# Kernel optimization log

Hardware: AMD Instinct MI355X
Metric: run time of the kernel (lower is better)

The kernel has to match this reference:

```python
import jax, jax.numpy as jnp
import numpy as np

HEADS = 8
DIM_HEAD = 64
CHUNK = 128
EPS = 1e-6
KERNEL_EPS = 1e-4


def softmax_kernel(x, proj, is_query):
    # x: [b,h,n,d], proj: [f,d]  (FAVOR+ positive softmax features)
    d = x.shape[-1]
    data_normalizer = d ** -0.25
    ratio = proj.shape[0] ** -0.5
    data_dash = jnp.einsum('bhnd,fd->bhnf', x * data_normalizer, proj)
    diag = 0.5 * (data_normalizer ** 2) * jnp.sum(x * x, axis=-1, keepdims=True)  # [b,h,n,1]
    if is_query:
        m = jnp.max(data_dash, axis=-1, keepdims=True)
    else:
        m = jnp.max(data_dash, axis=(-1, -2), keepdims=True)
    return ratio * (jnp.exp(data_dash - diag - jax.lax.stop_gradient(m)) + KERNEL_EPS)


def infer_hidden_states(q, k, v, chunk_size=CHUNK):
    # q,k: [b,h,n,f], v: [b,h,n,e]; chunked causal linear attention with carried cumsums
    b, h, n, f = q.shape
    e = v.shape[-1]
    nc = n // chunk_size

    def to_chunks(t):
        return jnp.moveaxis(t.reshape(b, h, nc, chunk_size, t.shape[-1]), 2, 0)

    qs, ks, vs = to_chunks(q), to_chunks(k), to_chunks(v)

    def step(carry, inp):
        Z, S = carry  # [b,h,1,f], [b,h,1,f,e]
        qc, kc, vc = inp
        k_cum = Z + jnp.cumsum(kc, axis=2)                       # [b,h,c,f]
        D_inv = 1.0 / jnp.einsum('bhnf,bhnf->bhn', qc, k_cum + EPS)
        ctx = jnp.einsum('bhnf,bhne->bhnfe', kc, vc)             # [b,h,c,f,e]
        ctx_cum = S + jnp.cumsum(ctx, axis=2)
        out = jnp.einsum('bhnfe,bhnf,bhn->bhne', ctx_cum, qc, D_inv)
        return (k_cum[:, :, -1:], ctx_cum[:, :, -1:]), out

    init = (jnp.zeros((b, h, 1, f), q.dtype), jnp.zeros((b, h, 1, f, e), q.dtype))
    (Z, S), outs = jax.lax.scan(step, init, (qs, ks, vs))
    out = jnp.moveaxis(outs, 0, 2).reshape(b, h, n, e)
    return out, Z[:, :, 0], S[:, :, 0]


def reference(x, proj, Wq, Wk, Wv, Wo, bo):
    b, n, dim = x.shape
    h, dh = HEADS, DIM_HEAD

    def split_heads(t):
        return jnp.transpose(t.reshape(b, n, h, dh), (0, 2, 1, 3))

    q = split_heads(x @ Wq)
    k = split_heads(x @ Wk)
    v = split_heads(x @ Wv)

    qf = softmax_kernel(q, proj, is_query=True)
    kf = softmax_kernel(k, proj, is_query=False)

    out, Z, S = infer_hidden_states(qf, kf, v)
    out = jnp.transpose(out, (0, 2, 1, 3)).reshape(b, n, h * dh)
    out = out @ Wo + bo
    return out, Z, S


def setup_inputs() -> dict:
    key = jax.random.key(0)
    ks = jax.random.split(key, 6)
    b, n, dim = 2, 2048, 512
    f = 256
    return {
        'x': jax.random.normal(ks[0], (b, n, dim), jnp.float32),
        'proj': jax.random.normal(ks[1], (f, DIM_HEAD), jnp.float32),
        'Wq': jax.random.normal(ks[2], (dim, dim), jnp.float32) * (dim ** -0.5),
        'Wk': jax.random.normal(ks[3], (dim, dim), jnp.float32) * (dim ** -0.5),
        'Wv': jax.random.normal(ks[4], (dim, dim), jnp.float32) * (dim ** -0.5),
        'Wo': jax.random.normal(ks[5], (dim, dim), jnp.float32) * (dim ** -0.5),
        'bo': jnp.zeros((dim,), jnp.float32),
    }
```

## Files before the change

kernel.cpp:

```cpp
#include <hip/hip_runtime.h>
#include <hip/hip_bf16.h>
#include <math.h>

#define NB    2
#define NSEQ  2048
#define DIMM  512
#define NH    8
#define DHd   64
#define FF    256
#define CHK   128
#define NCHK  16
#define NBH   16

typedef unsigned short ushort_t;
typedef __attribute__((ext_vector_type(8))) __bf16 bf16x8;
typedef __attribute__((ext_vector_type(4))) float floatx4;

__device__ __forceinline__ unsigned short f2bf(float x) {
    union { __hip_bfloat16 h; unsigned short u; } v;
    v.h = __float2bfloat16(x);
    return v.u;
}
__device__ __forceinline__ float bf2f(unsigned short u) {
    union { unsigned short u2[2]; float f; } v;
    v.u2[0] = 0; v.u2[1] = u;
    return v.f;
}
__device__ __forceinline__ unsigned enc_f(float x) {
    unsigned u = __float_as_uint(x);
    return (u & 0x80000000u) ? ~u : (u | 0x80000000u);
}
__device__ __forceinline__ float dec_f(unsigned e) {
    unsigned u = (e & 0x80000000u) ? (e & 0x7fffffffu) : ~e;
    return __uint_as_float(u);
}

__device__ __forceinline__ void gload16(const void* g, void* l) {
    __builtin_amdgcn_global_load_lds(
        (const __attribute__((address_space(1))) void*)g,
        (__attribute__((address_space(3))) void*)l, 16, 0, 0);
}

__device__ __forceinline__ bf16x8 frag8(const ushort_t* lds, int row, int kb) {
    return *((const bf16x8*)lds + row * 8 + (kb ^ (row & 7)));
}
__device__ __forceinline__ bf16x8 fragS(const ushort_t* lds, int row, int kb) {
    return *((const bf16x8*)lds + row * 16 + (kb ^ (row & 15)));
}

__device__ __forceinline__ void stage8(const ushort_t* __restrict__ G, ushort_t* dst,
                                       int ld, int tid) {
#pragma unroll
    for (int t = 0; t < 4; t++) {
        const int g = t * 256 + tid, r = g >> 3, kb = (g & 7) ^ (r & 7);
        gload16(G + (size_t)r * ld + kb * 8, dst + (size_t)g * 8);
    }
}
__device__ __forceinline__ void stage4h(const ushort_t* __restrict__ G, ushort_t* dst,
                                        int ld, int tid) {
#pragma unroll
    for (int t = 0; t < 2; t++) {
        const int g = t * 256 + tid, r = g >> 3, kb = (g & 7) ^ (r & 7);
        gload16(G + (size_t)r * ld + kb * 8, dst + (size_t)g * 8);
    }
}
__device__ __forceinline__ void stageV(const ushort_t* __restrict__ G, ushort_t* dst,
                                       int tid) {
#pragma unroll
    for (int t = 0; t < 4; t++) {
        const int g = t * 256 + tid, r = g >> 4, kb = (g & 15) ^ (r & 15);
        gload16(G + (size_t)r * NSEQ + kb * 8, dst + (size_t)g * 8);
    }
}

__global__ __launch_bounds__(256)
void prep(const float* __restrict__ x, const float* __restrict__ proj,
          const float* __restrict__ W0, const float* __restrict__ W1,
          const float* __restrict__ W2, const float* __restrict__ W3,
          ushort_t* __restrict__ xb, ushort_t* __restrict__ projb,
          ushort_t* __restrict__ T0, ushort_t* __restrict__ T1,
          ushort_t* __restrict__ T2, ushort_t* __restrict__ T3,
          unsigned* __restrict__ mk_u)
{
    __shared__ float t[32][33];
    const int b = blockIdx.x, tid = threadIdx.x;
    if (b < 2048) {
        const int gid = b * 256 + tid;
        const float4 v = *(const float4*)(x + (size_t)gid * 4);
        union { ushort4 v4; unsigned short s[4]; } pk;
        pk.s[0] = f2bf(v.x); pk.s[1] = f2bf(v.y); pk.s[2] = f2bf(v.z); pk.s[3] = f2bf(v.w);
        ((ushort4*)xb)[gid] = pk.v4;
    } else if (b < 2064) {
        const int gid = (b - 2048) * 256 + tid;
        const float dn = 0.35355339059327379f;
        const float4 v = *(const float4*)(proj + (size_t)gid * 4);
        union { ushort4 v4; unsigned short s[4]; } pk;
        pk.s[0] = f2bf(v.x * dn); pk.s[1] = f2bf(v.y * dn);
        pk.s[2] = f2bf(v.z * dn); pk.s[3] = f2bf(v.w * dn);
        ((ushort4*)projb)[gid] = pk.v4;
    } else if (b < 3088) {
        const int idx = b - 2064;
        const int z = idx >> 8, rem = idx & 255;
        const int bx = rem & 15, by = rem >> 4;
        const float* W = (z == 0) ? W0 : (z == 1) ? W1 : (z == 2) ? W2 : W3;
        ushort_t* T = (z == 0) ? T0 : (z == 1) ? T1 : (z == 2) ? T2 : T3;
        const int x0 = bx * 32, y0 = by * 32;
        const int tx = tid & 31, ty = tid >> 5;
#pragma unroll
        for (int i = 0; i < 4; i++)
            t[ty + i * 8][tx] = W[(size_t)(y0 + ty + i * 8) * DIMM + x0 + tx];
        __syncthreads();
#pragma unroll
        for (int i = 0; i < 4; i++)
            T[(size_t)(x0 + ty + i * 8) * DIMM + y0 + tx] = f2bf(t[tx][ty + i * 8]);
    } else {
        if (tid < NBH) mk_u[tid] = 0u;
    }
}

__device__ __forceinline__ void mfma_mainloop(
    const ushort_t* __restrict__ AG, const ushort_t* __restrict__ BG,
    ushort_t* As, ushort_t* Bs, int ldA, int ldB, int K,
    floatx4 acc[4][4], int tid)
{
    const int lane = tid & 63, wid = tid >> 6;
    const int q = lane >> 4, c = lane & 15;
    const int wm = (wid >> 1) * 64, wn = (wid & 1) * 64;

    for (int k0 = 0; k0 < K; k0 += 64) {
#pragma unroll
        for (int t = 0; t < 4; t++) {
            const int g = t * 256 + tid, r = g >> 3, kb = (g & 7) ^ (r & 7);
            gload16(AG + (size_t)r * ldA + k0 + kb * 8, As + (size_t)g * 8);
        }
#pragma unroll
        for (int t = 0; t < 4; t++) {
            const int g = t * 256 + tid, r = g >> 3, kb = (g & 7) ^ (r & 7);
            gload16(BG + (size_t)r * ldB + k0 + kb * 8, Bs + (size_t)g * 8);
        }
        __syncthreads();
#pragma unroll
        for (int ks = 0; ks < 2; ks++) {
            bf16x8 af[4], bfr[4];
#pragma unroll
            for (int i = 0; i < 4; i++) {
                af[i]  = frag8(As, wm + i * 16 + c, ks * 4 + q);
                bfr[i] = frag8(Bs, wn + i * 16 + c, ks * 4 + q);
            }
#pragma unroll
            for (int i = 0; i < 4; i++)
#pragma unroll
                for (int j = 0; j < 4; j++)
                    acc[i][j] = __builtin_amdgcn_mfma_f32_16x16x32_bf16(
                        af[i], bfr[j], acc[i][j], 0, 0, 0);
        }
        __syncthreads();
    }
}

__global__ __launch_bounds__(256)
void gemm_qkv(const ushort_t* __restrict__ xb,
              const ushort_t* __restrict__ Wtq, const ushort_t* __restrict__ Wtk,
              const ushort_t* __restrict__ Wtv, const ushort_t* __restrict__ projb,
              ushort_t* __restrict__ qb, ushort_t* __restrict__ kb,
              ushort_t* __restrict__ vTb, unsigned* __restrict__ mk_u)
{
    __shared__ alignas(16) ushort_t SM[25600];
    __shared__ float red[256];
    ushort_t* As = SM;
    ushort_t* Bs = SM + 8192;
    ushort_t* PS = SM + 17408;
    const int tid = threadIdx.x;
    const int bid = blockIdx.x;
    const int z = bid % 3, tt = bid / 3;
    const int n0 = (tt & 3) * 128, m0 = (tt >> 2) * 128;
    const ushort_t* Bt = (z == 0) ? Wtq : ((z == 1) ? Wtk : Wtv);

    floatx4 zero = {0.f, 0.f, 0.f, 0.f};
    floatx4 acc[4][4];
#pragma unroll
    for (int i = 0; i < 4; i++)
#pragma unroll
        for (int j = 0; j < 4; j++) acc[i][j] = zero;

    mfma_mainloop(xb + (size_t)m0 * DIMM, Bt + (size_t)n0 * DIMM, As, Bs,
                  DIMM, DIMM, DIMM, acc, tid);

    const int lane = tid & 63, wid = tid >> 6;
    const int q = lane >> 4, cl = lane & 15;
    const int wm = (wid >> 1) * 64, wn = (wid & 1) * 64;

#pragma unroll
    for (int i = 0; i < 4; i++)
#pragma unroll
        for (int j = 0; j < 4; j++) {
            const int col = wn + j * 16 + cl;
#pragma unroll
            for (int r = 0; r < 4; r++) {
                const int row = wm + i * 16 + q * 4 + r;
                SM[row * 136 + col] = f2bf(acc[i][j][r]);
            }
        }
    __syncthreads();

    if (z < 2) {
        ushort_t* ob = (z == 0) ? qb : kb;
        if (z == 1) {
#pragma unroll
            for (int t = 0; t < 4; t++) {
                const int g = t * 256 + tid, f = g >> 3, kbg = (g & 7) ^ (f & 7);
                gload16(projb + (size_t)f * 64 + kbg * 8, PS + (size_t)g * 8);
            }
        }
#pragma unroll
        for (int p = 0; p < 16; p++) {
            const int idx = p * 256 + tid;
            const int row = idx >> 5, c4 = idx & 31;
            ushort4 o = *(const ushort4*)&SM[row * 136 + c4 * 4];
            *(ushort4*)(ob + (size_t)(m0 + row) * DIMM + n0 + c4 * 4) = o;
        }
        if (z == 1) {
            const int bb = m0 >> 11;
            const int h0 = n0 >> 6;
            float mx[2] = {-3.0e38f, -3.0e38f};
#pragma unroll
            for (int half = 0; half < 2; half++) {
                __syncthreads();
#pragma unroll
                for (int hh = 0; hh < 2; hh++) {
                    floatx4 a2[4][4];
#pragma unroll
                    for (int i = 0; i < 4; i++)
#pragma unroll
                        for (int j = 0; j < 4; j++) a2[i][j] = zero;
#pragma unroll
                    for (int ks = 0; ks < 2; ks++) {
                        bf16x8 af[4], bfr[4];
#pragma unroll
                        for (int i = 0; i < 4; i++)
                            af[i] = *(const bf16x8*)&SM[(wm + i * 16 + cl) * 136 + hh * 64 + (ks * 4 + q) * 8];
#pragma unroll
                        for (int j = 0; j < 4; j++)
                            bfr[j] = frag8(PS, wn + j * 16 + cl, ks * 4 + q);
#pragma unroll
                        for (int i = 0; i < 4; i++)
#pragma unroll
                            for (int j = 0; j < 4; j++)
                                a2[i][j] = __builtin_amdgcn_mfma_f32_16x16x32_bf16(
                                    af[i], bfr[j], a2[i][j], 0, 0, 0);
                    }
#pragma unroll
                    for (int i = 0; i < 4; i++)
#pragma unroll
                        for (int j = 0; j < 4; j++)
#pragma unroll
                            for (int r = 0; r < 4; r++) mx[hh] = fmaxf(mx[hh], a2[i][j][r]);
                }
                if (half == 0) {
                    __syncthreads();
#pragma unroll
                    for (int t = 0; t < 4; t++) {
                        const int g = t * 256 + tid, f = g >> 3, kbg = (g & 7) ^ (f & 7);
                        gload16(projb + (size_t)(128 + f) * 64 + kbg * 8, PS + (size_t)g * 8);
                    }
                }
            }
#pragma unroll
            for (int hh = 0; hh < 2; hh++) {
                __syncthreads();
                red[tid] = mx[hh];
                __syncthreads();
                for (int s = 128; s > 0; s >>= 1) {
                    if (tid < s) red[tid] = fmaxf(red[tid], red[tid + s]);
                    __syncthreads();
                }
                if (tid == 0) atomicMax(&mk_u[bb * NH + h0 + hh], enc_f(red[0]));
            }
        }
    } else {
        const int bb = m0 >> 11, nbase = m0 & 2047;
#pragma unroll
        for (int p = 0; p < 16; p++) {
            const int idx = p * 256 + tid;
            const int cl2 = idx >> 5, n4 = idx & 31;
            const int C = n0 + cl2;
            const int h = C >> 6, e = C & 63;
            union { ushort4 v4; unsigned short s[4]; } pk;
#pragma unroll
            for (int k = 0; k < 4; k++) pk.s[k] = SM[(n4 * 4 + k) * 136 + cl2];
            *(ushort4*)(vTb + (((size_t)(bb * NH + h) * 64 + e)) * NSEQ + nbase + n4 * 4) = pk.v4;
        }
    }
}

__device__ __forceinline__ void mm24(const ushort_t* A, const ushort_t* B,
                                     floatx4 acc[2][4], int wm, int wn, int c, int q)
{
#pragma unroll
    for (int ks = 0; ks < 2; ks++) {
        bf16x8 af[2], bfr[4];
#pragma unroll
        for (int i = 0; i < 2; i++) af[i] = frag8(A, wm + i * 16 + c, ks * 4 + q);
#pragma unroll
        for (int j = 0; j < 4; j++) bfr[j] = frag8(B, wn + j * 16 + c, ks * 4 + q);
#pragma unroll
        for (int i = 0; i < 2; i++)
#pragma unroll
            for (int j = 0; j < 4; j++)
                acc[i][j] = __builtin_amdgcn_mfma_f32_16x16x32_bf16(
                    af[i], bfr[j], acc[i][j], 0, 0, 0);
    }
}

__global__ __launch_bounds__(256)
void gemm_out(const ushort_t* __restrict__ attnb, const ushort_t* __restrict__ Wto,
              float* __restrict__ out, const float* __restrict__ bias)
{
    __shared__ alignas(16) ushort_t A0[4096];
    __shared__ alignas(16) ushort_t A1[4096];
    __shared__ alignas(16) ushort_t B0[8192];
    __shared__ alignas(16) ushort_t B1[8192];
    const int tid = threadIdx.x;
    const int n0 = blockIdx.x * 128, m0 = blockIdx.y * 64;
    const ushort_t* AG = attnb + (size_t)m0 * DIMM;
    const ushort_t* BG = Wto + (size_t)n0 * DIMM;

    floatx4 zero = {0.f, 0.f, 0.f, 0.f};
    floatx4 acc[2][4];
#pragma unroll
    for (int i = 0; i < 2; i++)
#pragma unroll
        for (int j = 0; j < 4; j++) acc[i][j] = zero;

    const int lane = tid & 63, wid = tid >> 6;
    const int q = lane >> 4, c = lane & 15;
    const int wm = (wid >> 1) * 32, wn = (wid & 1) * 64;

    stage4h(AG, A0, DIMM, tid);
    stage8(BG, B0, DIMM, tid);
    __syncthreads();
    for (int tt = 0; tt < 4; tt++) {
        const int k0 = tt * 128;
        stage4h(AG + k0 + 64, A1, DIMM, tid);
        stage8(BG + k0 + 64, B1, DIMM, tid);
        mm24(A0, B0, acc, wm, wn, c, q);
        __syncthreads();
        if (tt < 3) {
            stage4h(AG + k0 + 128, A0, DIMM, tid);
            stage8(BG + k0 + 128, B0, DIMM, tid);
        }
        mm24(A1, B1, acc, wm, wn, c, q);
        __syncthreads();
    }

#pragma unroll
    for (int i = 0; i < 2; i++)
#pragma unroll
        for (int j = 0; j < 4; j++) {
            const int col = n0 + wn + j * 16 + c;
            const float bv = bias[col];
#pragma unroll
            for (int r = 0; r < 4; r++) {
                const int row = m0 + wm + i * 16 + q * 4 + r;
                out[(size_t)row * DIMM + col] = acc[i][j][r] + bv;
            }
        }
}

__global__ __launch_bounds__(256)
void featk(const ushort_t* __restrict__ kb_, const ushort_t* __restrict__ projb,
           const unsigned* __restrict__ mk_u, const ushort_t* __restrict__ vTb,
           ushort_t* __restrict__ kfb, float* __restrict__ CTXT,
           float* __restrict__ Ksum)
{
    __shared__ alignas(16) ushort_t SM[17408];
    __shared__ alignas(16) ushort_t Vs[8192];
    __shared__ float dtmp[256];
    __shared__ float diag_l[128];
    __shared__ float colp[2][128];
    ushort_t* As = SM;
    ushort_t* Bs = SM + 8192;
    const int tid = threadIdx.x, lane = tid & 63, wid = tid >> 6;
    const int q = lane >> 4, cl = lane & 15;
    const int m0 = blockIdx.x * 128, h = blockIdx.y, fh = blockIdx.z;
    const int bb = m0 >> 11, nloc = m0 & 2047;
    const int bh = bb * NH + h;
    const int cidx = nloc >> 7;
    const ushort_t* Aq = kb_ + (size_t)m0 * DIMM + h * 64;
    const ushort_t* Vg = vTb + ((size_t)bh * 64) * NSEQ + nloc;
    const ushort_t* Pj = projb + (size_t)fh * 128 * 64;

    {
        const int row = tid >> 1, half = tid & 1;
        float s = 0.f;
        const ushort_t* p = Aq + (size_t)row * DIMM + half * 32;
#pragma unroll
        for (int d = 0; d < 32; d += 4) {
            ushort4 w = *(const ushort4*)(p + d);
            float a = bf2f(w.x), b2 = bf2f(w.y), c2 = bf2f(w.z), d2 = bf2f(w.w);
            s += a * a + b2 * b2 + c2 * c2 + d2 * d2;
        }
        dtmp[tid] = s;
    }
    stage8(Aq, As, DIMM, tid);
    stage8(Pj, Bs, 64, tid);
    stageV(Vg, Vs, tid);
    __syncthreads();
    if (tid < 128) diag_l[tid] = (dtmp[2 * tid] + dtmp[2 * tid + 1]) * 0.0625f;

    floatx4 zero = {0.f, 0.f, 0.f, 0.f};
    floatx4 acc[4][4];
#pragma unroll
    for (int i = 0; i < 4; i++)
#pragma unroll
        for (int j = 0; j < 4; j++) acc[i][j] = zero;
    const int wm = (wid >> 1) * 64, wn = (wid & 1) * 64;
#pragma unroll
    for (int ks = 0; ks < 2; ks++) {
        bf16x8 af[4], bfr[4];
#pragma unroll
        for (int i = 0; i < 4; i++) af[i] = frag8(As, wm + i * 16 + cl, ks * 4 + q);
#pragma unroll
        for (int j = 0; j < 4; j++) bfr[j] = frag8(Bs, wn + j * 16 + cl, ks * 4 + q);
#pragma unroll
        for (int i = 0; i < 4; i++)
#pragma unroll
            for (int j = 0; j < 4; j++)
                acc[i][j] = __builtin_amdgcn_mfma_f32_16x16x32_bf16(
                    af[i], bfr[j], acc[i][j], 0, 0, 0);
    }
    __syncthreads();

    const float mk = dec_f(mk_u[bh]);
#pragma unroll
    for (int i = 0; i < 4; i++)
#pragma unroll
        for (int r = 0; r < 4; r++) {
            const int row = wm + i * 16 + q * 4 + r;
            const float cc = diag_l[row] + mk;
#pragma unroll
            for (int j = 0; j < 4; j++)
                acc[i][j][r] = 0.0625f * (__expf(acc[i][j][r] - cc) + 1.0e-4f);
        }

#pragma unroll
    for (int j = 0; j < 4; j++) {
        float s = 0.f;
#pragma unroll
        for (int i = 0; i < 4; i++)
            s += acc[i][j][0] + acc[i][j][1] + acc[i][j][2] + acc[i][j][3];
        s += __shfl_xor(s, 16);
        s += __shfl_xor(s, 32);
        if (q == 0) colp[wid >> 1][wn + j * 16 + cl] = s;
    }

#pragma unroll
    for (int i = 0; i < 4; i++)
#pragma unroll
        for (int j = 0; j < 4; j++) {
            const int col = wn + j * 16 + cl;
#pragma unroll
            for (int r = 0; r < 4; r++) {
                const int row = wm + i * 16 + q * 4 + r;
                SM[row * 136 + col] = f2bf(acc[i][j][r]);
            }
        }
    __syncthreads();

    if (tid < 128)
        Ksum[((size_t)bh * NCHK + cidx) * FF + fh * 128 + tid] = colp[0][tid] + colp[1][tid];

    const size_t frow = (size_t)bh * NSEQ + nloc;
#pragma unroll
    for (int p = 0; p < 16; p++) {
        const int idx = p * 256 + tid;
        const int row = idx >> 5, c4 = idx & 31;
        ushort4 o = *(const ushort4*)&SM[row * 136 + c4 * 4];
        *(ushort4*)(kfb + (frow + row) * FF + fh * 128 + c4 * 4) = o;
    }
    __syncthreads();

    ushort_t* T = SM;
    const size_t cbase = ((size_t)bh * NCHK + cidx) * 64;
#pragma unroll
    for (int fq = 0; fq < 2; fq++) {
        if ((wid & 1) == fq) {
#pragma unroll
            for (int jj = 0; jj < 4; jj++) {
#pragma unroll
                for (int i = 0; i < 4; i++)
#pragma unroll
                    for (int r = 0; r < 4; r++) {
                        const int n = wm + i * 16 + q * 4 + r;
                        T[(jj * 16 + cl) * 136 + n] = f2bf(acc[i][jj][r]);
                    }
            }
        }
        __syncthreads();
        floatx4 accc[4];
#pragma unroll
        for (int jj = 0; jj < 4; jj++) accc[jj] = zero;
#pragma unroll
        for (int kt = 0; kt < 4; kt++) {
            const bf16x8 av = fragS(Vs, wid * 16 + cl, kt * 4 + q);
#pragma unroll
            for (int jj = 0; jj < 4; jj++) {
                const bf16x8 bv = *(const bf16x8*)(T + (jj * 16 + cl) * 136 + (kt * 4 + q) * 8);
                accc[jj] = __builtin_amdgcn_mfma_f32_16x16x32_bf16(av, bv, accc[jj], 0, 0, 0);
            }
        }
#pragma unroll
        for (int jj = 0; jj < 4; jj++) {
            const int f = fh * 128 + fq * 64 + jj * 16 + cl;
#pragma unroll
            for (int r = 0; r < 4; r++) {
                const int e = wid * 16 + q * 4 + r;
                CTXT[(cbase + e) * FF + f] = accc[jj][r];
            }
        }
        __syncthreads();
    }
}

__global__ void prefix_zs(float* __restrict__ Ksum, float* __restrict__ Zout,
                          const float* __restrict__ CTXT, ushort_t* __restrict__ ctxp,
                          float* __restrict__ Sout)
{
    const int b = blockIdx.x;
    if (b < 1024) {
        const int idx = b * 256 + threadIdx.x;
        const int bh = idx >> 14, ef = idx & 16383;
        const int e = ef >> 8, f = ef & 255;
        float run = 0.f;
#pragma unroll
        for (int c = 0; c < NCHK; c++) {
            const size_t o = (((size_t)bh * NCHK + c) * 64 + e) * FF + f;
            const float t = CTXT[o];
            ctxp[o] = f2bf(run);
            run += t;
        }
        Sout[((size_t)bh * FF + f) * 64 + e] = run;
    } else {
        const int idx = (b - 1024) * 256 + threadIdx.x;
        const int bh = idx >> 8, f = idx & 255;
        float run = 0.f;
#pragma unroll
        for (int c = 0; c < NCHK; c++) {
            const size_t o = ((size_t)(bh * NCHK + c)) * FF + f;
            const float t = Ksum[o];
            Ksum[o] = run;
            run += t;
        }
        Zout[(size_t)bh * FF + f] = run;
    }
}

template<int NJ>
__device__ __forceinline__ void st1N(const ushort_t* QFs, const ushort_t* Bk,
                                     floatx4* acc1, int wv, int cl, int q)
{
#pragma unroll
    for (int ks = 0; ks < 2; ks++) {
        const bf16x8 af = frag8(QFs, wv * 16 + cl, ks * 4 + q);
        bf16x8 bfr[NJ];
#pragma unroll
        for (int j = 0; j < NJ; j++) bfr[j] = frag8(Bk, j * 16 + cl, ks * 4 + q);
#pragma unroll
        for (int j = 0; j < NJ; j++)
            acc1[j] = __builtin_amdgcn_mfma_f32_16x16x32_bf16(af, bfr[j], acc1[j], 0, 0, 0);
    }
}

__device__ __forceinline__ void pv4(const ushort_t* CpB, const ushort_t* QFs,
                                    floatx4 acc2[4], int wv, int cl, int q)
{
#pragma unroll
    for (int ks = 0; ks < 2; ks++) {
        const bf16x8 bfr = frag8(QFs, wv * 16 + cl, ks * 4 + q);
#pragma unroll
        for (int i = 0; i < 4; i++) {
            const bf16x8 af = frag8(CpB, i * 16 + cl, ks * 4 + q);
            acc2[i] = __builtin_amdgcn_mfma_f32_16x16x32_bf16(af, bfr, acc2[i], 0, 0, 0);
        }
    }
}

__global__ __launch_bounds__(256)
void chunk_out_half(const ushort_t* __restrict__ qb_, const ushort_t* __restrict__ projb,
                    const ushort_t* __restrict__ kfb, const ushort_t* __restrict__ vTb,
                    const float* __restrict__ Zex, const ushort_t* __restrict__ ctxp,
                    ushort_t* __restrict__ attnb)
{
    __shared__ alignas(16) ushort_t QF[16384];
    __shared__ alignas(16) ushort_t BufA[8192];
    __shared__ alignas(16) ushort_t Ssl[8192];
    __shared__ alignas(16) ushort_t BufB[4096];
    __shared__ float zeps[256];
    __shared__ float dtmp[256];
    __shared__ float diag_l[64];
    __shared__ float rows_part[64];
    __shared__ float denp[256];
    __shared__ float den_l[64];

    const int tid = threadIdx.x, lane = tid & 63, wv = tid >> 6;
    const int q = lane >> 4, cl = lane & 15;
    const int bh = blockIdx.x >> 5, r5 = blockIdx.x & 31;
    const int c = r5 >> 1, hq = r5 & 1;
    const int bb = bh >> 3, h = bh & 7;
    const int n0 = c * CHK, q0 = n0 + hq * 64;
    const ushort_t* Kf = kfb + ((size_t)bh * NSEQ + n0) * FF;
    const ushort_t* Aq = qb_ + ((size_t)(bb * NSEQ + q0)) * DIMM + h * 64;
    const ushort_t* Vt = vTb + ((size_t)bh * 64) * NSEQ + n0;
    const ushort_t* Cp = ctxp + ((size_t)bh * NCHK + c) * 64 * FF;

    zeps[tid] = Zex[((size_t)bh * NCHK + c) * FF + tid] + 1.0e-6f;

    stage4h(Aq, BufB, DIMM, tid);
    stage8(projb, BufA, 64, tid);
    stage8(projb + 128 * 64, Ssl, 64, tid);
    {
        const int row = tid >> 2, qd = tid & 3;
        float s = 0.f;
        const ushort_t* p = Aq + (size_t)row * DIMM + qd * 16;
#pragma unroll
        for (int d = 0; d < 16; d += 4) {
            ushort4 w = *(const ushort4*)(p + d);
            float a = bf2f(w.x), b2 = bf2f(w.y), c2 = bf2f(w.z), d2 = bf2f(w.w);
            s += a * a + b2 * b2 + c2 * c2 + d2 * d2;
        }
        dtmp[tid] = s;
    }
    __syncthreads();
    if (tid < 64)
        diag_l[tid] = (dtmp[4 * tid] + dtmp[4 * tid + 1] +
                       dtmp[4 * tid + 2] + dtmp[4 * tid + 3]) * 0.0625f;

    floatx4 zero = {0.f, 0.f, 0.f, 0.f};
    floatx4 accqA[8], accqB[8];
#pragma unroll
    for (int j = 0; j < 8; j++) { accqA[j] = zero; accqB[j] = zero; }
#pragma unroll
    for (int ks = 0; ks < 2; ks++) {
        const bf16x8 af = frag8(BufB, wv * 16 + cl, ks * 4 + q);
#pragma unroll
        for (int j = 0; j < 8; j++) {
            const bf16x8 b0 = frag8(BufA, j * 16 + cl, ks * 4 + q);
            accqA[j] = __builtin_amdgcn_mfma_f32_16x16x32_bf16(af, b0, accqA[j], 0, 0, 0);
        }
#pragma unroll
        for (int j = 0; j < 8; j++) {
            const bf16x8 b1 = frag8(Ssl, j * 16 + cl, ks * 4 + q);
            accqB[j] = __builtin_amdgcn_mfma_f32_16x16x32_bf16(af, b1, accqB[j], 0, 0, 0);
        }
    }
    float rmax[4];
#pragma unroll
    for (int r = 0; r < 4; r++) {
        float m = -3.0e38f;
#pragma unroll
        for (int j = 0; j < 8; j++) m = fmaxf(m, fmaxf(accqA[j][r], accqB[j][r]));
        m = fmaxf(m, __shfl_xor(m, 1)); m = fmaxf(m, __shfl_xor(m, 2));
        m = fmaxf(m, __shfl_xor(m, 4)); m = fmaxf(m, __shfl_xor(m, 8));
        rmax[r] = m;
    }
    __syncthreads();
#pragma unroll
    for (int r = 0; r < 4; r++) {
        const int rowL = wv * 16 + q * 4 + r;
        const float cc = diag_l[rowL] + rmax[r];
#pragma unroll
        for (int j = 0; j < 8; j++) {
            {
                const int col = j * 16 + cl;
                const float v = 0.0625f * (__expf(accqA[j][r] - cc) + 1.0e-4f);
                const int s = col >> 6, fp = col & 63;
                QF[s * 4096 + (rowL * 8 + ((fp >> 3) ^ (rowL & 7))) * 8 + (fp & 7)] = f2bf(v);
            }
            {
                const int col = 128 + j * 16 + cl;
                const float v = 0.0625f * (__expf(accqB[j][r] - cc) + 1.0e-4f);
                const int s = col >> 6, fp = col & 63;
                QF[s * 4096 + (rowL * 8 + ((fp >> 3) ^ (rowL & 7))) * 8 + (fp & 7)] = f2bf(v);
            }
        }
    }
    if (hq) stage8(Kf, Ssl, FF, tid); else stage4h(Kf, Ssl, FF, tid);
    __syncthreads();

    floatx4 acc1[8];
#pragma unroll
    for (int j = 0; j < 8; j++) acc1[j] = zero;
    if (hq) {
        stage8(Kf + 64, BufA, FF, tid);
        st1N<8>(QF, Ssl, acc1, wv, cl, q);
        __syncthreads();
        stage8(Kf + 128, Ssl, FF, tid);
        st1N<8>(QF + 4096, BufA, acc1, wv, cl, q);
        __syncthreads();
        stage8(Kf + 192, BufA, FF, tid);
        st1N<8>(QF + 8192, Ssl, acc1, wv, cl, q);
        __syncthreads();
        st1N<8>(QF + 12288, BufA, acc1, wv, cl, q);
    } else {
        stage4h(Kf + 64, BufA, FF, tid);
        st1N<4>(QF, Ssl, acc1, wv, cl, q);
        __syncthreads();
        stage4h(Kf + 128, Ssl, FF, tid);
        st1N<4>(QF + 4096, BufA, acc1, wv, cl, q);
        __syncthreads();
        stage4h(Kf + 192, BufA, FF, tid);
        st1N<4>(QF + 8192, Ssl, acc1, wv, cl, q);
        __syncthreads();
        st1N<4>(QF + 12288, BufA, acc1, wv, cl, q);
    }

    if (hq) {
#pragma unroll
        for (int r = 0; r < 4; r++) {
            const int rowL = wv * 16 + q * 4 + r;
            const int rowG = 64 + rowL;
            float part = 0.f;
#pragma unroll
            for (int j = 0; j < 8; j++) {
                const int col = j * 16 + cl;
                const float v = (col <= rowG) ? acc1[j][r] : 0.f;
                part += v;
                Ssl[(rowL * 16 + ((col >> 3) ^ (rowL & 15))) * 8 + (col & 7)] = f2bf(v);
            }
            part += __shfl_xor(part, 1); part += __shfl_xor(part, 2);
            part += __shfl_xor(part, 4); part += __shfl_xor(part, 8);
            if (cl == 0) rows_part[rowL] = part;
        }
    } else {
#pragma unroll
        for (int r = 0; r < 4; r++) {
            const int rowL = wv * 16 + q * 4 + r;
            float part = 0.f;
#pragma unroll
            for (int j = 0; j < 4; j++) {
                const int col = j * 16 + cl;
                const float v = (col <= rowL) ? acc1[j][r] : 0.f;
                part += v;
                Ssl[(rowL * 16 + ((col >> 3) ^ (rowL & 15))) * 8 + (col & 7)] = f2bf(v);
            }
            part += __shfl_xor(part, 1); part += __shfl_xor(part, 2);
            part += __shfl_xor(part, 4); part += __shfl_xor(part, 8);
            if (cl == 0) rows_part[rowL] = part;
        }
    }
    __syncthreads();

    if (hq) stageV(Vt, BufA, tid); else stage4h(Vt, BufA, NSEQ, tid);
    stage4h(Cp, BufB, FF, tid);
    float dacc = 0.f;
    {
        const int drow = tid >> 2, dq = tid & 3;
        const ushort_t* QQ = QF + dq * 4096;
#pragma unroll
        for (int gi = 0; gi < 8; gi++) {
            const ushort_t* gp = QQ + ((size_t)drow * 8 + (gi ^ (drow & 7))) * 8;
            const int kbase = dq * 64 + gi * 8;
#pragma unroll
            for (int e2 = 0; e2 < 8; e2++)
                dacc = fmaf(bf2f(gp[e2]), zeps[kbase + e2], dacc);
        }
    }
    __syncthreads();

    floatx4 acc2[4];
#pragma unroll
    for (int i = 0; i < 4; i++) acc2[i] = zero;
    if (hq) {
#pragma unroll
        for (int kk = 0; kk < 4; kk++) {
            const bf16x8 bfr = fragS(Ssl, wv * 16 + cl, kk * 4 + q);
#pragma unroll
            for (int i = 0; i < 4; i++) {
                const bf16x8 af = fragS(BufA, i * 16 + cl, kk * 4 + q);
                acc2[i] = __builtin_amdgcn_mfma_f32_16x16x32_bf16(af, bfr, acc2[i], 0, 0, 0);
            }
        }
    } else {
#pragma unroll
        for (int kk = 0; kk < 2; kk++) {
            const bf16x8 bfr = fragS(Ssl, wv * 16 + cl, kk * 4 + q);
#pragma unroll
            for (int i = 0; i < 4; i++) {
                const bf16x8 af = frag8(BufA, i * 16 + cl, kk * 4 + q);
                acc2[i] = __builtin_amdgcn_mfma_f32_16x16x32_bf16(af, bfr, acc2[i], 0, 0, 0);
            }
        }
    }
    denp[tid] = dacc;
    __syncthreads();

    stage4h(Cp + 64, BufA, FF, tid);
    stage4h(Cp + 128, BufA + 4096, FF, tid);
    pv4(BufB, QF, acc2, wv, cl, q);
    __syncthreads();
    stage4h(Cp + 192, BufB, FF, tid);
    pv4(BufA, QF + 4096, acc2, wv, cl, q);
    pv4(BufA + 4096, QF + 8192, acc2, wv, cl, q);
    if (tid < 64)
        den_l[tid] = rows_part[tid] + denp[4 * tid] + denp[4 * tid + 1] +
                     denp[4 * tid + 2] + denp[4 * tid + 3];
    __syncthreads();
    pv4(BufB, QF + 12288, acc2, wv, cl, q);

    const float dinv = 1.0f / den_l[wv * 16 + cl];
#pragma unroll
    for (int i = 0; i < 4; i++)
#pragma unroll
        for (int r = 0; r < 4; r++) {
            const int e = i * 16 + q * 4 + r;
            Ssl[(wv * 16 + cl) * 68 + e] = f2bf(acc2[i][r] * dinv);
        }
    __syncthreads();
#pragma unroll
    for (int p = 0; p < 4; p++) {
        const int idx = p * 256 + tid;
        const int row = idx >> 4, e4 = idx & 15;
        ushort4 o = *(const ushort4*)&Ssl[row * 68 + e4 * 4];
        *(ushort4*)(attnb + ((size_t)(bb * NSEQ + q0 + row)) * DIMM + h * 64 + e4 * 4) = o;
    }
}

extern "C" void kernel_launch(void* const* d_in, const int* in_sizes, int n_in,
                              void* d_out, int out_size, void* d_ws, size_t ws_size,
                              hipStream_t stream)
{
    (void)in_sizes; (void)n_in; (void)out_size; (void)ws_size;
    const float* x    = (const float*)d_in[0];
    const float* proj = (const float*)d_in[1];
    const float* Wq   = (const float*)d_in[2];
    const float* Wk   = (const float*)d_in[3];
    const float* Wv   = (const float*)d_in[4];
    const float* Wo   = (const float*)d_in[5];
    const float* bo   = (const float*)d_in[6];
    float* out = (float*)d_out;

    char* W = (char*)d_ws;
    float*    CTXT = (float*)W;              W += (size_t)16777216;
    ushort_t* kfb  = (ushort_t*)W;           W += (size_t)16777216;
    ushort_t* ctxp = (ushort_t*)W;           W += (size_t)8388608;
    ushort_t* qb   = (ushort_t*)W;           W += (size_t)4194304;
    ushort_t* kb   = (ushort_t*)W;           W += (size_t)4194304;
    ushort_t* xb   = (ushort_t*)W;           W += (size_t)4194304;
    ushort_t* vTb  = (ushort_t*)W;           W += (size_t)4194304;
    ushort_t* Wtq  = (ushort_t*)W;           W += (size_t)524288;
    ushort_t* Wtk  = (ushort_t*)W;           W += (size_t)524288;
    ushort_t* Wtv  = (ushort_t*)W;           W += (size_t)524288;
    ushort_t* Wto  = (ushort_t*)W;           W += (size_t)524288;
    ushort_t* projb = (ushort_t*)W;          W += (size_t)32768;
    float*    Ksum = (float*)W;              W += (size_t)262144;
    unsigned* mk_u = (unsigned*)W;           W += (size_t)256;

    ushort_t* attnb = xb;

    float* Zout = out + (size_t)4096 * 512;
    float* Sout = Zout + (size_t)NBH * FF;

    hipLaunchKernelGGL(prep, dim3(3089), dim3(256), 0, stream,
                       x, proj, Wq, Wk, Wv, Wo, xb, projb, Wtq, Wtk, Wtv, Wto, mk_u);
    hipLaunchKernelGGL(gemm_qkv, dim3(384), dim3(256), 0, stream,
                       xb, Wtq, Wtk, Wtv, projb, qb, kb, vTb, mk_u);
    hipLaunchKernelGGL(featk, dim3(32, 8, 2), dim3(256), 0, stream,
                       kb, projb, mk_u, vTb, kfb, CTXT, Ksum);
    hipLaunchKernelGGL(prefix_zs, dim3(1040), dim3(256), 0, stream,
                       Ksum, Zout, CTXT, ctxp, Sout);
    hipLaunchKernelGGL(chunk_out_half, dim3(512), dim3(256), 0, stream,
                       qb, projb, kfb, vTb, Ksum, ctxp, attnb);
    hipLaunchKernelGGL(gemm_out, dim3(4, 64), dim3(256), 0, stream, attnb, Wto, out, bo);
}
```

Baseline: 135.3 us.

## Double-buffer QKV GEMM mainloop and replace block reduction with warp shuffles

The QKV projection GEMM now ping-pongs between two shared-memory tile buffers, so global loads for the next K-slice are issued while MFMAs run on the current one. Both halves of the feature projection matrix are loaded into shared memory in one go after the mainloop, which removes the mid-loop barrier and reload. The max reduction for the key features switches from a tree of shared-memory barriers to wave shuffles plus a small per-wave array. The cost is more shared memory per block, which may lower occupancy.

```diff
diff --git a/kernel.cpp b/kernel.cpp
--- a/kernel.cpp
+++ b/kernel.cpp
@@ -118,43 +118,23 @@
     }
 }
 
-__device__ __forceinline__ void mfma_mainloop(
-    const ushort_t* __restrict__ AG, const ushort_t* __restrict__ BG,
-    ushort_t* As, ushort_t* Bs, int ldA, int ldB, int K,
-    floatx4 acc[4][4], int tid)
-{
-    const int lane = tid & 63, wid = tid >> 6;
-    const int q = lane >> 4, c = lane & 15;
-    const int wm = (wid >> 1) * 64, wn = (wid & 1) * 64;
-
-    for (int k0 = 0; k0 < K; k0 += 64) {
-#pragma unroll
-        for (int t = 0; t < 4; t++) {
-            const int g = t * 256 + tid, r = g >> 3, kb = (g & 7) ^ (r & 7);
-            gload16(AG + (size_t)r * ldA + k0 + kb * 8, As + (size_t)g * 8);
-        }
-#pragma unroll
-        for (int t = 0; t < 4; t++) {
-            const int g = t * 256 + tid, r = g >> 3, kb = (g & 7) ^ (r & 7);
-            gload16(BG + (size_t)r * ldB + k0 + kb * 8, Bs + (size_t)g * 8);
-        }
-        __syncthreads();
-#pragma unroll
-        for (int ks = 0; ks < 2; ks++) {
-            bf16x8 af[4], bfr[4];
-#pragma unroll
-            for (int i = 0; i < 4; i++) {
-                af[i]  = frag8(As, wm + i * 16 + c, ks * 4 + q);
-                bfr[i] = frag8(Bs, wn + i * 16 + c, ks * 4 + q);
-            }
-#pragma unroll
-            for (int i = 0; i < 4; i++)
-#pragma unroll
-                for (int j = 0; j < 4; j++)
-                    acc[i][j] = __builtin_amdgcn_mfma_f32_16x16x32_bf16(
-                        af[i], bfr[j], acc[i][j], 0, 0, 0);
-        }
-        __syncthreads();
+__device__ __forceinline__ void mm44(const ushort_t* A, const ushort_t* B,
+                                     floatx4 acc[4][4], int wm, int wn, int c, int q)
+{
+#pragma unroll
+    for (int ks = 0; ks < 2; ks++) {
+        bf16x8 af[4], bfr[4];
+#pragma unroll
+        for (int i = 0; i < 4; i++) {
+            af[i]  = frag8(A, wm + i * 16 + c, ks * 4 + q);
+            bfr[i] = frag8(B, wn + i * 16 + c, ks * 4 + q);
+        }
+#pragma unroll
+        for (int i = 0; i < 4; i++)
+#pragma unroll
+            for (int j = 0; j < 4; j++)
+                acc[i][j] = __builtin_amdgcn_mfma_f32_16x16x32_bf16(
+                    af[i], bfr[j], acc[i][j], 0, 0, 0);
     }
 }
 
@@ -165,31 +145,54 @@
               ushort_t* __restrict__ qb, ushort_t* __restrict__ kb,
               ushort_t* __restrict__ vTb, unsigned* __restrict__ mk_u)
 {
-    __shared__ alignas(16) ushort_t SM[25600];
-    __shared__ float red[256];
-    ushort_t* As = SM;
-    ushort_t* Bs = SM + 8192;
+    __shared__ alignas(16) ushort_t SM[33792];
+    __shared__ float wred[2][4];
+    ushort_t* A0 = SM;
+    ushort_t* B0 = SM + 8192;
+    ushort_t* A1 = SM + 16384;
+    ushort_t* B1 = SM + 24576;
     ushort_t* PS = SM + 17408;
     const int tid = threadIdx.x;
     const int bid = blockIdx.x;
     const int z = bid % 3, tt = bid / 3;
     const int n0 = (tt & 3) * 128, m0 = (tt >> 2) * 128;
     const ushort_t* Bt = (z == 0) ? Wtq : ((z == 1) ? Wtk : Wtv);
-
-    floatx4 zero = {0.f, 0.f, 0.f, 0.f};
-    floatx4 acc[4][4];
-#pragma unroll
-    for (int i = 0; i < 4; i++)
-#pragma unroll
-        for (int j = 0; j < 4; j++) acc[i][j] = zero;
-
-    mfma_mainloop(xb + (size_t)m0 * DIMM, Bt + (size_t)n0 * DIMM, As, Bs,
-                  DIMM, DIMM, DIMM, acc, tid);
+    const ushort_t* AG = xb + (size_t)m0 * DIMM;
+    const ushort_t* BG = Bt + (size_t)n0 * DIMM;
 
     const int lane = tid & 63, wid = tid >> 6;
     const int q = lane >> 4, cl = lane & 15;
     const int wm = (wid >> 1) * 64, wn = (wid & 1) * 64;
 
+    floatx4 zero = {0.f, 0.f, 0.f, 0.f};
+    floatx4 acc[4][4];
+#pragma unroll
+    for (int i = 0; i < 4; i++)
+#pragma unroll
+        for (int j = 0; j < 4; j++) acc[i][j] = zero;
+
+    stage8(AG, A0, DIMM, tid);
+    stage8(BG, B0, DIMM, tid);
+    __syncthreads();
+    for (int t4 = 0; t4 < 4; t4++) {
+        const int k0 = t4 * 128;
+        stage8(AG + k0 + 64, A1, DIMM, tid);
+        stage8(BG + k0 + 64, B1, DIMM, tid);
+        mm44(A0, B0, acc, wm, wn, cl, q);
+        __syncthreads();
+        if (t4 < 3) {
+            stage8(AG + k0 + 128, A0, DIMM, tid);
+            stage8(BG + k0 + 128, B0, DIMM, tid);
+        }
+        mm44(A1, B1, acc, wm, wn, cl, q);
+        __syncthreads();
+    }
+
+    if (z == 1) {
+        stage8(projb, PS, 64, tid);
+        stage8(projb + 8192, PS + 8192, 64, tid);
+    }
+
 #pragma unroll
     for (int i = 0; i < 4; i++)
 #pragma unroll
@@ -205,13 +208,6 @@
 
     if (z < 2) {
         ushort_t* ob = (z == 0) ? qb : kb;
-        if (z == 1) {
-#pragma unroll
-            for (int t = 0; t < 4; t++) {
-                const int g = t * 256 + tid, f = g >> 3, kbg = (g & 7) ^ (f & 7);
-                gload16(projb + (size_t)f * 64 + kbg * 8, PS + (size_t)g * 8);
-            }
-        }
 #pragma unroll
         for (int p = 0; p < 16; p++) {
             const int idx = p * 256 + tid;
@@ -224,10 +220,9 @@
             const int h0 = n0 >> 6;
             float mx[2] = {-3.0e38f, -3.0e38f};
 #pragma unroll
-            for (int half = 0; half < 2; half++) {
-                __syncthreads();
-#pragma unroll
-                for (int hh = 0; hh < 2; hh++) {
+            for (int hh = 0; hh < 2; hh++) {
+#pragma unroll
+                for (int half = 0; half < 2; half++) {
                     floatx4 a2[4][4];
 #pragma unroll
                     for (int i = 0; i < 4; i++)
@@ -241,7 +236,7 @@
                             af[i] = *(const bf16x8*)&SM[(wm + i * 16 + cl) * 136 + hh * 64 + (ks * 4 + q) * 8];
 #pragma unroll
                         for (int j = 0; j < 4; j++)
-                            bfr[j] = frag8(PS, wn + j * 16 + cl, ks * 4 + q);
+                            bfr[j] = frag8(PS + half * 8192, wn + j * 16 + cl, ks * 4 + q);
 #pragma unroll
                         for (int i = 0; i < 4; i++)
 #pragma unroll
@@ -256,25 +251,23 @@
 #pragma unroll
                             for (int r = 0; r < 4; r++) mx[hh] = fmaxf(mx[hh], a2[i][j][r]);
                 }
-                if (half == 0) {
-                    __syncthreads();
-#pragma unroll
-                    for (int t = 0; t < 4; t++) {
-                        const int g = t * 256 + tid, f = g >> 3, kbg = (g & 7) ^ (f & 7);
-                        gload16(projb + (size_t)(128 + f) * 64 + kbg * 8, PS + (size_t)g * 8);
-                    }
+            }
+#pragma unroll
+            for (int hh = 0; hh < 2; hh++) {
+                float m = mx[hh];
+                m = fmaxf(m, __shfl_xor(m, 1));  m = fmaxf(m, __shfl_xor(m, 2));
+                m = fmaxf(m, __shfl_xor(m, 4));  m = fmaxf(m, __shfl_xor(m, 8));
+                m = fmaxf(m, __shfl_xor(m, 16)); m = fmaxf(m, __shfl_xor(m, 32));
+                if (lane == 0) wred[hh][wid] = m;
+            }
+            __syncthreads();
+            if (tid == 0) {
+#pragma unroll
+                for (int hh = 0; hh < 2; hh++) {
+                    const float m = fmaxf(fmaxf(wred[hh][0], wred[hh][1]),
+                                          fmaxf(wred[hh][2], wred[hh][3]));
+                    atomicMax(&mk_u[bb * NH + h0 + hh], enc_f(m));
                 }
-            }
-#pragma unroll
-            for (int hh = 0; hh < 2; hh++) {
-                __syncthreads();
-                red[tid] = mx[hh];
-                __syncthreads();
-                for (int s = 128; s > 0; s >>= 1) {
-                    if (tid < s) red[tid] = fmaxf(red[tid], red[tid + s]);
-                    __syncthreads();
-                }
-                if (tid == 0) atomicMax(&mk_u[bb * NH + h0 + hh], enc_f(red[0]));
             }
         }
     } else {
```

Result: no change. 135.3 us (+0.0%).
